# Performance work log

Measured on AMD Instinct MI355X. Metric: run time of the kernel, lower is better.

Reference implementation:

```python
import jax, jax.numpy as jnp
import numpy as np

N = 4096       # n_stocks
D = 256        # input_dim
O = 256        # output_dim
C = 3          # adjacency channels (weight rows = input_dim + 3)


def setup_inputs() -> dict:
    key = jax.random.key(0)
    k1, k2, k3, k4 = jax.random.split(key, 4)
    adjacency = jax.random.uniform(k1, (N, N, C), dtype=jnp.float32)
    input_feature = jax.random.normal(k2, (N, D), dtype=jnp.float32)
    Beta = jax.random.uniform(k3, (N, N), dtype=jnp.float32)
    # xavier-uniform for weight [D+C, O]
    limit = float(np.sqrt(6.0 / (D + C + O)))
    weight = jax.random.uniform(k4, (D + C, O), minval=-limit, maxval=limit,
                                dtype=jnp.float32)
    bias = jnp.zeros((O,), dtype=jnp.float32)
    return {"adjacency": adjacency, "input_feature": input_feature,
            "Beta": Beta, "weight": weight, "bias": bias}


def reference(adjacency, input_feature, Beta, weight, bias):
    # Original per-target loop:
    #   source_y = concat([input_feature, adjacency[:, y, :]], axis=1)  # [N, D+C]
    #   u_y      = source_y @ weight                                    # [N, O]
    #   out[y]   = Beta[:, y] @ u_y                                     # [O]
    # Split weight into feature part Wf [D, O] and adjacency part Wa [C, O].
    # out = Beta^T @ (X @ Wf) + (sum_n Beta[n, y] * adjacency[n, y, :]) @ Wa
    d = input_feature.shape[1]
    Wf = weight[:d]            # [D, O]
    Wa = weight[d:]            # [C, O]
    feat_term = Beta.T @ (input_feature @ Wf)                     # [N, O]
    adj_agg = jnp.einsum('ny,nyc->yc', Beta, adjacency)           # [N, C]
    out = feat_term + adj_agg @ Wa + bias                         # [N, O]
    return out
```

## Files before the change

kernel.cpp:

```cpp
#include <hip/hip_runtime.h>
#include <hip/hip_bf16.h>

#define NN 4096
#define DD 256
#define OO 256
#define NR 8
#define ROWF (NN * 3)
#define NSPLIT 8
#define NAGG 32
#define NB2 (NN / NR)

typedef __attribute__((ext_vector_type(4))) float f32x4;
typedef __attribute__((ext_vector_type(8))) short bf16x8;
typedef __attribute__((ext_vector_type(8))) short short8;
typedef __attribute__((ext_vector_type(4))) unsigned int u32x4;
typedef __attribute__((ext_vector_type(2))) unsigned int u32x2;

__device__ __forceinline__ short f2bfs(float f) {
    __hip_bfloat16 h = __float2bfloat16(f);
    short s;
    __builtin_memcpy(&s, &h, 2);
    return s;
}

__device__ __forceinline__ float bfs2f(unsigned short u) {
    unsigned int v = (unsigned int)u << 16;
    float f;
    __builtin_memcpy(&f, &v, 4);
    return f;
}

__device__ __forceinline__ unsigned pack2(float a, float b) {
    return (unsigned)(unsigned short)f2bfs(a)
         | ((unsigned)(unsigned short)f2bfs(b) << 16);
}

__global__ __launch_bounds__(256) void k1_xwt(
    const float* __restrict__ X, const float* __restrict__ W,
    unsigned short* __restrict__ XWTb)
{
    __shared__ float xs[8][DD];
    const int t = threadIdx.x;
    const int m0 = blockIdx.x * 8;

    #pragma unroll
    for (int i = 0; i < 8; ++i)
        xs[i][t] = X[(size_t)(m0 + i) * DD + t];
    __syncthreads();

    float acc[8];
    #pragma unroll
    for (int m = 0; m < 8; ++m) acc[m] = 0.f;

    for (int k0 = 0; k0 < DD; k0 += 4) {
        float w0 = W[(size_t)(k0 + 0) * OO + t];
        float w1 = W[(size_t)(k0 + 1) * OO + t];
        float w2 = W[(size_t)(k0 + 2) * OO + t];
        float w3 = W[(size_t)(k0 + 3) * OO + t];
        #pragma unroll
        for (int m = 0; m < 8; ++m) {
            const f32x4 xv = *reinterpret_cast<const f32x4*>(&xs[m][k0]);
            acc[m] = fmaf(xv[0], w0, acc[m]);
            acc[m] = fmaf(xv[1], w1, acc[m]);
            acc[m] = fmaf(xv[2], w2, acc[m]);
            acc[m] = fmaf(xv[3], w3, acc[m]);
        }
    }

    unsigned int p[4];
    #pragma unroll
    for (int i = 0; i < 4; ++i)
        p[i] = pack2(acc[2 * i], acc[2 * i + 1]);
    unsigned short* dst = XWTb
        + ((((size_t)(m0 >> 3) * (OO / 16) + (t >> 4)) * 16) + (t & 15)) * 8;
    *reinterpret_cast<u32x4*>(dst) = (u32x4){p[0], p[1], p[2], p[3]};
}

__global__ __launch_bounds__(1024, 8) void k2_stream(
    const float* __restrict__ Adj, const float* __restrict__ Beta,
    unsigned short* __restrict__ apart)
{
    __shared__ unsigned short bsm16[NR * NN];
    const int t = threadIdx.x;
    const int nb = blockIdx.x;
    const int n0 = nb * NR;

    int fpos[3], y0[3], rr[3];
    #pragma unroll
    for (int p = 0; p < 3; ++p) {
        fpos[p] = p * NN + 4 * t;
        y0[p] = fpos[p] / 3;
        rr[p] = fpos[p] - 3 * y0[p];
    }

    f32x4 br[NR];
    #pragma unroll
    for (int n = 0; n < NR; ++n)
        br[n] = *reinterpret_cast<const f32x4*>(Beta + (size_t)(n0 + n) * NN + 4 * t);

    #pragma unroll
    for (int n = 0; n < NR; ++n) {
        const unsigned lo = pack2(br[n][0], br[n][1]);
        const unsigned hi = pack2(br[n][2], br[n][3]);
        *reinterpret_cast<u32x2*>(&bsm16[n * NN + 4 * t]) = (u32x2){lo, hi};
    }
    __syncthreads();

    f32x4 acc[3];
    #pragma unroll
    for (int p = 0; p < 3; ++p) acc[p] = (f32x4){0.f, 0.f, 0.f, 0.f};

    const float* arow = Adj + (size_t)n0 * ROWF;
    #pragma unroll 1
    for (int n = 0; n < NR; ++n) {
        f32x4 av[3];
        #pragma unroll
        for (int p = 0; p < 3; ++p)
            av[p] = __builtin_nontemporal_load(
                reinterpret_cast<const f32x4*>(arow + fpos[p]));
        #pragma unroll
        for (int p = 0; p < 3; ++p) {
            const float bl = bfs2f(bsm16[n * NN + y0[p]]);
            const float bh = bfs2f(bsm16[n * NN + y0[p] + 1]);
            #pragma unroll
            for (int q = 0; q < 4; ++q) {
                const float w = (rr[p] + q < 3) ? bl : bh;
                acc[p][q] = fmaf(w, av[p][q], acc[p][q]);
            }
        }
        arow += ROWF;
    }

    unsigned short* op = apart + (size_t)nb * ROWF;
    #pragma unroll
    for (int p = 0; p < 3; ++p) {
        const unsigned lo = pack2(acc[p][0], acc[p][1]);
        const unsigned hi = pack2(acc[p][2], acc[p][3]);
        *reinterpret_cast<u32x2*>(op + fpos[p]) = (u32x2){lo, hi};
    }
}

__global__ __launch_bounds__(256) void k2b_reduce(
    const unsigned short* __restrict__ apart, float* __restrict__ agg2)
{
    const int t = threadIdx.x;
    const int i0 = blockIdx.x * 2048 + t * 8;
    const int g = blockIdx.y;

    float s[8];
    #pragma unroll
    for (int j = 0; j < 8; ++j) s[j] = 0.f;

    #pragma unroll 4
    for (int r = 0; r < NB2 / NAGG; ++r) {
        const short8 v = *reinterpret_cast<const short8*>(
            apart + (size_t)(g * (NB2 / NAGG) + r) * ROWF + i0);
        #pragma unroll
        for (int j = 0; j < 8; ++j)
            s[j] += bfs2f((unsigned short)v[j]);
    }

    float* d = agg2 + (size_t)g * ROWF + i0;
    *reinterpret_cast<f32x4*>(d)     = (f32x4){s[0], s[1], s[2], s[3]};
    *reinterpret_cast<f32x4*>(d + 4) = (f32x4){s[4], s[5], s[6], s[7]};
}

__global__ __launch_bounds__(256) void k4_gemm(
    const float* __restrict__ Beta, const unsigned short* __restrict__ XWTb,
    unsigned short* __restrict__ gpart, int clen)
{
    const int t = threadIdx.x;
    const int lane = t & 63;
    const int w = t >> 6;
    const int g16 = lane >> 4, r16 = lane & 15;
    const int y0 = blockIdx.x * 64 + 16 * w;
    const int sp = blockIdx.y;
    const int nb = sp * clen;
    const int ksteps = clen / 32;

    f32x4 acc[16];
    #pragma unroll
    for (int f = 0; f < 16; ++f) acc[f] = (f32x4){0.f, 0.f, 0.f, 0.f};

    const float* bp = Beta + (size_t)(nb + 8 * g16) * NN + (y0 + r16);

    float bcur[8];
    #pragma unroll
    for (int j = 0; j < 8; ++j)
        bcur[j] = bp[(size_t)j * NN];

    for (int kc = 0; kc < ksteps; ++kc) {
        bf16x8 av;
        #pragma unroll
        for (int j = 0; j < 8; ++j)
            av[j] = f2bfs(bcur[j]);

        if (kc + 1 < ksteps) {
            const float* bn = bp + (size_t)(kc + 1) * 32 * NN;
            #pragma unroll
            for (int j = 0; j < 8; ++j)
                bcur[j] = bn[(size_t)j * NN];
        }

        const int mc = ((nb >> 3) + kc * 4) + g16;
        const unsigned short* xb = XWTb + (((size_t)mc * 16) * 16 + r16) * 8;
        #pragma unroll
        for (int f = 0; f < 16; ++f) {
            const bf16x8 bv = *reinterpret_cast<const bf16x8*>(xb + (size_t)f * 128);
            acc[f] = __builtin_amdgcn_mfma_f32_16x16x32_bf16(av, bv, acc[f], 0, 0, 0);
        }
    }

    unsigned short* gp = gpart + (size_t)sp * NN * OO;
    #pragma unroll
    for (int f = 0; f < 16; ++f) {
        const int o = 16 * f + r16;
        #pragma unroll
        for (int r = 0; r < 4; ++r)
            gp[(size_t)(y0 + 4 * g16 + r) * OO + o] = (unsigned short)f2bfs(acc[f][r]);
    }
}

__global__ __launch_bounds__(256) void k3_final(
    const unsigned short* __restrict__ gpart, const float* __restrict__ agg2,
    const float* __restrict__ W, const float* __restrict__ bias,
    float* __restrict__ Out)
{
    __shared__ float af[8][3];
    const int t = threadIdx.x;
    const int yb = blockIdx.x * 8;

    if (t < 24) {
        const int yl = t / 3, c = t % 3;
        float s = 0.f;
        #pragma unroll
        for (int g = 0; g < NAGG; ++g)
            s += agg2[(size_t)g * ROWF + (yb + yl) * 3 + c];
        af[yl][c] = s;
    }
    __syncthreads();

    const int idx = blockIdx.x * 256 + t;
    const int y = idx >> 5;
    const int o0 = (idx & 31) * 8;
    const int yl = y & 7;

    float s[8];
    #pragma unroll
    for (int j = 0; j < 8; ++j) s[j] = 0.f;
    #pragma unroll
    for (int sp = 0; sp < NSPLIT; ++sp) {
        const short8 v = *reinterpret_cast<const short8*>(
            gpart + (size_t)sp * NN * OO + (size_t)y * OO + o0);
        #pragma unroll
        for (int j = 0; j < 8; ++j)
            s[j] += bfs2f((unsigned short)v[j]);
    }

    const float a0 = af[yl][0], a1 = af[yl][1], a2 = af[yl][2];
    float r[8];
    #pragma unroll
    for (int j = 0; j < 8; ++j) {
        const int oo = o0 + j;
        r[j] = s[j] + a0 * W[(size_t)(DD + 0) * OO + oo]
                    + a1 * W[(size_t)(DD + 1) * OO + oo]
                    + a2 * W[(size_t)(DD + 2) * OO + oo]
                    + bias[oo];
    }
    float* od = Out + (size_t)y * OO + o0;
    *reinterpret_cast<f32x4*>(od)     = (f32x4){r[0], r[1], r[2], r[3]};
    *reinterpret_cast<f32x4*>(od + 4) = (f32x4){r[4], r[5], r[6], r[7]};
}

extern "C" void kernel_launch(void* const* d_in, const int* in_sizes, int n_in,
                              void* d_out, int out_size, void* d_ws, size_t ws_size,
                              hipStream_t stream) {
    (void)in_sizes; (void)n_in; (void)out_size; (void)ws_size;
    const float* adj  = (const float*)d_in[0];
    const float* X    = (const float*)d_in[1];
    const float* Beta = (const float*)d_in[2];
    const float* W    = (const float*)d_in[3];
    const float* bias = (const float*)d_in[4];
    float* out = (float*)d_out;

    const size_t xwt_b   = (size_t)OO * NN * 2;
    const size_t gpart_b = (size_t)NSPLIT * NN * OO * 2;
    const size_t apart_b = (size_t)NB2 * ROWF * 2;

    char* p = (char*)d_ws;
    unsigned short* XWTb   = (unsigned short*)p;            p += xwt_b;
    unsigned short* gpart  = (unsigned short*)p;            p += gpart_b;
    unsigned short* apart  = (unsigned short*)p;            p += apart_b;
    float*          agg2   = (float*)p;

    const int clen = NN / NSPLIT;

    k1_xwt<<<dim3(NN / 8), dim3(256), 0, stream>>>(X, W, XWTb);
    k2_stream<<<dim3(NB2), dim3(1024), 0, stream>>>(adj, Beta, apart);
    k2b_reduce<<<dim3(6, NAGG), dim3(256), 0, stream>>>(apart, agg2);
    k4_gemm<<<dim3(NN / 64, NSPLIT), dim3(256), 0, stream>>>(Beta, XWTb, gpart, clen);
    k3_final<<<dim3(NN / 8), dim3(256), 0, stream>>>(gpart, agg2, W, bias, out);
}
```

Measured before the change: 119.3 us.

## Fuse adjacency streaming and Beta GEMM into one interleaved heterogeneous kernel

Merges the bandwidth-bound adjacency aggregation kernel and the MFMA Beta^T·XW GEMM into a single launch. Even blocks do adjacency streaming and odd blocks do GEMM tiles, which are now 1024-thread blocks where each of 16 waves covers a 16x64 output slice. The aim is to overlap the memory-heavy stream with the compute-heavy GEMM and remove one launch. In exchange, GEMM blocks inherit the large shared-memory allocation and 1024-thread launch bounds, which may limit occupancy, and the GEMM reloads Beta per output quarter.

After: 99.13 us (median of 2 runs). 16.9% less time.

```diff
diff --git a/kernel.cpp b/kernel.cpp
--- a/kernel.cpp
+++ b/kernel.cpp
@@ -76,67 +76,125 @@
     *reinterpret_cast<u32x4*>(dst) = (u32x4){p[0], p[1], p[2], p[3]};
 }
 
-__global__ __launch_bounds__(1024, 8) void k2_stream(
+__global__ __launch_bounds__(1024, 8) void k24(
     const float* __restrict__ Adj, const float* __restrict__ Beta,
-    unsigned short* __restrict__ apart)
+    const unsigned short* __restrict__ XWTb,
+    unsigned short* __restrict__ apart, unsigned short* __restrict__ gpart)
 {
     __shared__ unsigned short bsm16[NR * NN];
     const int t = threadIdx.x;
-    const int nb = blockIdx.x;
-    const int n0 = nb * NR;
-
-    int fpos[3], y0[3], rr[3];
-    #pragma unroll
-    for (int p = 0; p < 3; ++p) {
-        fpos[p] = p * NN + 4 * t;
-        y0[p] = fpos[p] / 3;
-        rr[p] = fpos[p] - 3 * y0[p];
-    }
-
-    f32x4 br[NR];
-    #pragma unroll
-    for (int n = 0; n < NR; ++n)
-        br[n] = *reinterpret_cast<const f32x4*>(Beta + (size_t)(n0 + n) * NN + 4 * t);
-
-    #pragma unroll
-    for (int n = 0; n < NR; ++n) {
-        const unsigned lo = pack2(br[n][0], br[n][1]);
-        const unsigned hi = pack2(br[n][2], br[n][3]);
-        *reinterpret_cast<u32x2*>(&bsm16[n * NN + 4 * t]) = (u32x2){lo, hi};
-    }
-    __syncthreads();
-
-    f32x4 acc[3];
-    #pragma unroll
-    for (int p = 0; p < 3; ++p) acc[p] = (f32x4){0.f, 0.f, 0.f, 0.f};
-
-    const float* arow = Adj + (size_t)n0 * ROWF;
-    #pragma unroll 1
-    for (int n = 0; n < NR; ++n) {
-        f32x4 av[3];
-        #pragma unroll
-        for (int p = 0; p < 3; ++p)
-            av[p] = __builtin_nontemporal_load(
-                reinterpret_cast<const f32x4*>(arow + fpos[p]));
+
+    if ((blockIdx.x & 1) == 0) {
+        const int nb = blockIdx.x >> 1;
+        const int n0 = nb * NR;
+
+        int fpos[3], y0[3], rr[3];
         #pragma unroll
         for (int p = 0; p < 3; ++p) {
-            const float bl = bfs2f(bsm16[n * NN + y0[p]]);
-            const float bh = bfs2f(bsm16[n * NN + y0[p] + 1]);
-            #pragma unroll
-            for (int q = 0; q < 4; ++q) {
-                const float w = (rr[p] + q < 3) ? bl : bh;
-                acc[p][q] = fmaf(w, av[p][q], acc[p][q]);
+            fpos[p] = p * NN + 4 * t;
+            y0[p] = fpos[p] / 3;
+            rr[p] = fpos[p] - 3 * y0[p];
+        }
+
+        f32x4 br[NR];
+        #pragma unroll
+        for (int n = 0; n < NR; ++n)
+            br[n] = *reinterpret_cast<const f32x4*>(Beta + (size_t)(n0 + n) * NN + 4 * t);
+
+        #pragma unroll
+        for (int n = 0; n < NR; ++n) {
+            const unsigned lo = pack2(br[n][0], br[n][1]);
+            const unsigned hi = pack2(br[n][2], br[n][3]);
+            *reinterpret_cast<u32x2*>(&bsm16[n * NN + 4 * t]) = (u32x2){lo, hi};
+        }
+        __syncthreads();
+
+        f32x4 acc[3];
+        #pragma unroll
+        for (int p = 0; p < 3; ++p) acc[p] = (f32x4){0.f, 0.f, 0.f, 0.f};
+
+        const float* arow = Adj + (size_t)n0 * ROWF;
+        #pragma unroll 1
+        for (int n = 0; n < NR; ++n) {
+            f32x4 av[3];
+            #pragma unroll
+            for (int p = 0; p < 3; ++p)
+                av[p] = __builtin_nontemporal_load(
+                    reinterpret_cast<const f32x4*>(arow + fpos[p]));
+            #pragma unroll
+            for (int p = 0; p < 3; ++p) {
+                const float bl = bfs2f(bsm16[n * NN + y0[p]]);
+                const float bh = bfs2f(bsm16[n * NN + y0[p] + 1]);
+                #pragma unroll
+                for (int q = 0; q < 4; ++q) {
+                    const float w = (rr[p] + q < 3) ? bl : bh;
+                    acc[p][q] = fmaf(w, av[p][q], acc[p][q]);
+                }
             }
-        }
-        arow += ROWF;
-    }
-
-    unsigned short* op = apart + (size_t)nb * ROWF;
-    #pragma unroll
-    for (int p = 0; p < 3; ++p) {
-        const unsigned lo = pack2(acc[p][0], acc[p][1]);
-        const unsigned hi = pack2(acc[p][2], acc[p][3]);
-        *reinterpret_cast<u32x2*>(op + fpos[p]) = (u32x2){lo, hi};
+            arow += ROWF;
+        }
+
+        unsigned short* op = apart + (size_t)nb * ROWF;
+        #pragma unroll
+        for (int p = 0; p < 3; ++p) {
+            const unsigned lo = pack2(acc[p][0], acc[p][1]);
+            const unsigned hi = pack2(acc[p][2], acc[p][3]);
+            *reinterpret_cast<u32x2*>(op + fpos[p]) = (u32x2){lo, hi};
+        }
+    } else {
+        const int kb = blockIdx.x >> 1;
+        const int sp = kb & (NSPLIT - 1);
+        const int by = kb >> 3;
+        const int lane = t & 63;
+        const int w = t >> 6;
+        const int wy = w >> 2, wo = w & 3;
+        const int g16 = lane >> 4, r16 = lane & 15;
+        const int y0 = by * 64 + wy * 16;
+        const int o0 = wo * 64;
+        const int nb4 = sp * (NN / NSPLIT);
+        const int ksteps = (NN / NSPLIT) / 32;
+
+        f32x4 acc[4];
+        #pragma unroll
+        for (int f = 0; f < 4; ++f) acc[f] = (f32x4){0.f, 0.f, 0.f, 0.f};
+
+        const float* bp = Beta + (size_t)(nb4 + 8 * g16) * NN + (y0 + r16);
+        float bcur[8];
+        #pragma unroll
+        for (int j = 0; j < 8; ++j)
+            bcur[j] = bp[(size_t)j * NN];
+
+        for (int kc = 0; kc < ksteps; ++kc) {
+            bf16x8 av;
+            #pragma unroll
+            for (int j = 0; j < 8; ++j)
+                av[j] = f2bfs(bcur[j]);
+
+            if (kc + 1 < ksteps) {
+                const float* bn = bp + (size_t)(kc + 1) * 32 * NN;
+                #pragma unroll
+                for (int j = 0; j < 8; ++j)
+                    bcur[j] = bn[(size_t)j * NN];
+            }
+
+            const int mc = ((nb4 >> 3) + kc * 4) + g16;
+            const unsigned short* xb = XWTb
+                + (((size_t)mc * 16 + (o0 >> 4)) * 16 + r16) * 8;
+            #pragma unroll
+            for (int f = 0; f < 4; ++f) {
+                const bf16x8 bv = *reinterpret_cast<const bf16x8*>(xb + (size_t)f * 128);
+                acc[f] = __builtin_amdgcn_mfma_f32_16x16x32_bf16(av, bv, acc[f], 0, 0, 0);
+            }
+        }
+
+        unsigned short* gp = gpart + (size_t)sp * NN * OO;
+        #pragma unroll
+        for (int f = 0; f < 4; ++f) {
+            const int o = o0 + 16 * f + r16;
+            #pragma unroll
+            for (int r = 0; r < 4; ++r)
+                gp[(size_t)(y0 + 4 * g16 + r) * OO + o] = (unsigned short)f2bfs(acc[f][r]);
+        }
     }
 }
 
@@ -163,62 +221,6 @@
     float* d = agg2 + (size_t)g * ROWF + i0;
     *reinterpret_cast<f32x4*>(d)     = (f32x4){s[0], s[1], s[2], s[3]};
     *reinterpret_cast<f32x4*>(d + 4) = (f32x4){s[4], s[5], s[6], s[7]};
-}
-
-__global__ __launch_bounds__(256) void k4_gemm(
-    const float* __restrict__ Beta, const unsigned short* __restrict__ XWTb,
-    unsigned short* __restrict__ gpart, int clen)
-{
-    const int t = threadIdx.x;
-    const int lane = t & 63;
-    const int w = t >> 6;
-    const int g16 = lane >> 4, r16 = lane & 15;
-    const int y0 = blockIdx.x * 64 + 16 * w;
-    const int sp = blockIdx.y;
-    const int nb = sp * clen;
-    const int ksteps = clen / 32;
-
-    f32x4 acc[16];
-    #pragma unroll
-    for (int f = 0; f < 16; ++f) acc[f] = (f32x4){0.f, 0.f, 0.f, 0.f};
-
-    const float* bp = Beta + (size_t)(nb + 8 * g16) * NN + (y0 + r16);
-
-    float bcur[8];
-    #pragma unroll
-    for (int j = 0; j < 8; ++j)
-        bcur[j] = bp[(size_t)j * NN];
-
-    for (int kc = 0; kc < ksteps; ++kc) {
-        bf16x8 av;
-        #pragma unroll
-        for (int j = 0; j < 8; ++j)
-            av[j] = f2bfs(bcur[j]);
-
-        if (kc + 1 < ksteps) {
-            const float* bn = bp + (size_t)(kc + 1) * 32 * NN;
-            #pragma unroll
-            for (int j = 0; j < 8; ++j)
-                bcur[j] = bn[(size_t)j * NN];
-        }
-
-        const int mc = ((nb >> 3) + kc * 4) + g16;
-        const unsigned short* xb = XWTb + (((size_t)mc * 16) * 16 + r16) * 8;
-        #pragma unroll
-        for (int f = 0; f < 16; ++f) {
-            const bf16x8 bv = *reinterpret_cast<const bf16x8*>(xb + (size_t)f * 128);
-            acc[f] = __builtin_amdgcn_mfma_f32_16x16x32_bf16(av, bv, acc[f], 0, 0, 0);
-        }
-    }
-
-    unsigned short* gp = gpart + (size_t)sp * NN * OO;
-    #pragma unroll
-    for (int f = 0; f < 16; ++f) {
-        const int o = 16 * f + r16;
-        #pragma unroll
-        for (int r = 0; r < 4; ++r)
-            gp[(size_t)(y0 + 4 * g16 + r) * OO + o] = (unsigned short)f2bfs(acc[f][r]);
-    }
 }
 
 __global__ __launch_bounds__(256) void k3_final(
@@ -293,11 +295,8 @@
     unsigned short* apart  = (unsigned short*)p;            p += apart_b;
     float*          agg2   = (float*)p;
 
-    const int clen = NN / NSPLIT;
-
     k1_xwt<<<dim3(NN / 8), dim3(256), 0, stream>>>(X, W, XWTb);
-    k2_stream<<<dim3(NB2), dim3(1024), 0, stream>>>(adj, Beta, apart);
+    k24<<<dim3(2 * NB2), dim3(1024), 0, stream>>>(adj, Beta, XWTb, apart, gpart);
     k2b_reduce<<<dim3(6, NAGG), dim3(256), 0, stream>>>(apart, agg2);
-    k4_gemm<<<dim3(NN / 64, NSPLIT), dim3(256), 0, stream>>>(Beta, XWTb, gpart, clen);
     k3_final<<<dim3(NN / 8), dim3(256), 0, stream>>>(gpart, agg2, W, bias, out);
 }
```
